# Kernel tuning notes

Hardware: AMD Instinct MI355X
Metric: run time of the kernel (lower is better)

## Reference

```python
import jax, jax.numpy as jnp
import numpy as np


def _make_constraint_mask(n=9):
    N = n * n
    rows = np.arange(N) // n
    cols = np.arange(N) % n
    box = (rows // 3) * 3 + cols // 3
    cm = np.stack([
        rows[:, None] == rows[None, :],
        cols[:, None] == cols[None, :],
        box[:, None] == box[None, :],
    ], axis=1).astype(np.float32)  # (N, 3, N)
    return cm


def setup_inputs() -> dict:
    n, H, B = 9, 100, 512
    N = n * n
    key = jax.random.key(0)
    k1, k2, k3, k4 = jax.random.split(key, 4)
    digits = jax.random.randint(k1, (B, N), 0, n)
    keep = jax.random.bernoulli(k2, 0.5, (B, N)).astype(jnp.float32)
    x = jax.nn.one_hot(digits, n, dtype=jnp.float32) * keep[..., None]
    constraint_mask = jnp.asarray(_make_constraint_mask(n))  # (81, 3, 81)
    W1 = jax.random.normal(k3, (H, 3 * n), jnp.float32) / np.sqrt(3 * n).astype(np.float32)
    W2 = jax.random.normal(k4, (n, H), jnp.float32) / np.sqrt(H).astype(np.float32)
    return {"x": x, "constraint_mask": constraint_mask, "W1": W1, "W2": W2}


def reference(x, constraint_mask, W1, W2):
    B, N, n = x.shape
    bidx = jnp.arange(B)

    def step(carry, _):
        x, x_pred = carry
        # sparse constraint aggregation: constraints[b,i,k,v] = sum_j cm[i,k,j] * x[b,j,v]
        constraints = jnp.einsum('ikj,bjv->bikv', constraint_mask, x)  # (B,N,3,n)
        empty = x.sum(-1) == 0  # (B,N) cells still unfilled
        f = constraints.reshape(B, N, 3 * n)
        s_ = jax.nn.softmax(jax.nn.relu(f @ W1.T) @ W2.T, axis=-1)  # (B,N,n)
        x_pred = jnp.where(empty[..., None], s_, x_pred)
        s = jnp.where(empty[..., None], s_, 0.0)
        score = s.max(-1)          # (B,N)
        pos = s.argmax(-1)         # (B,N) best digit per cell
        mmax = jnp.argmax(score, axis=1)  # (B,) most confident cell
        has_empty = empty.any(axis=1)     # rows with remaining empties get a write
        p = pos[bidx, mmax]
        old = x[bidx, mmax, p]
        x = x.at[bidx, mmax, p].set(jnp.where(has_empty, 1.0, old))
        return (x, x_pred), None

    # Original loops min_empty (= max empties in batch) times; iterations past a
    # row's fill point are exact no-ops, so a fixed N=n*n steps gives identical output.
    (x, x_pred), _ = jax.lax.scan(step, (x, x), None, length=N)
    return (x_pred, x)
```

## Files before the change

kernel.cpp:

```cpp
#include <hip/hip_runtime.h>
#include <math.h>


#define NCELL 81
#define ND 9
#define NH 100
#define NG 27
#define GP 12
#define NTHREADS 256

template<int OFF>
__device__ __forceinline__ float pt_dot(const float* __restrict__ gr,
                                        const float (&w1r)[NG], int bp)
{
    float g[9];
    float4 ga = *(const float4*)gr;
    float4 gb = *(const float4*)(gr + 4);
    g[0]=ga.x; g[1]=ga.y; g[2]=ga.z; g[3]=ga.w;
    g[4]=gb.x; g[5]=gb.y; g[6]=gb.z; g[7]=gb.w;
    g[8]=gr[8];
    float acc = 0.0f;
    #pragma unroll
    for (int v = 0; v < 9; ++v)
        acc = fmaf(w1r[OFF + v], g[v] + ((v == bp) ? 1.0f : 0.0f), acc);
    return acc;
}

__global__ __launch_bounds__(NTHREADS, 2)
void sudoku_solver_kernel(const float* __restrict__ x_in,
                          const float* __restrict__ W1,
                          const float* __restrict__ W2,
                          float* __restrict__ out,
                          int B)
{
    __shared__ float xs[NCELL * ND];
    __shared__ float xp[NCELL * ND];
    alignas(16) __shared__ float gsum[NG * GP];
    alignas(16) __shared__ float PT[NG * NH];
    alignas(16) __shared__ float hs[NCELL * NH];
    __shared__ float escore[NCELL];
    __shared__ int   epos[NCELL];
    __shared__ int   elist[NCELL];
    __shared__ int   wlist[NCELL];
    __shared__ int   EcntS, Wcnt;

    const int b   = blockIdx.x;
    const int tid = threadIdx.x;
    if (b >= B) return;

    const int lane = tid & 63;
    const int wv   = tid >> 6;
    const int sgrp = lane / 9;
    const int vd   = lane - 9 * sgrp;
    const int u    = tid % NH;
    const int sub  = tid / NH;

    float w1r[NG];
    if (tid < 2 * NH) {
        #pragma unroll
        for (int k = 0; k < NG; ++k) w1r[k] = W1[u * NG + k];
    }
    float4 w2r[25];
    {
        const float4* w2row = (const float4*)&W2[vd * NH];
        #pragma unroll
        for (int q = 0; q < 25; ++q) w2r[q] = w2row[q];
    }

    {
        const float* xb = x_in + (size_t)b * (NCELL * ND);
        for (int i = tid; i < NCELL * ND; i += NTHREADS) {
            float v = xb[i];
            xs[i] = v;
            xp[i] = v;
        }
    }
    if (tid == 0) EcntS = 0;
    __syncthreads();

    for (int t = tid; t < NCELL + NG * ND; t += NTHREADS) {
        if (t < NCELL) {
            const float* r = &xs[t * ND];
            float s = r[0]+r[1]+r[2]+r[3]+r[4]+r[5]+r[6]+r[7]+r[8];
            if (s == 0.0f) { int e = atomicAdd(&EcntS, 1); elist[e] = t; }
        } else {
            int g = (t - NCELL) / ND;
            int v = (t - NCELL) % ND;
            float acc = 0.0f;
            if (g < 9) {
                int base = g * 9;
                #pragma unroll
                for (int j = 0; j < 9; ++j) acc += xs[(base + j) * ND + v];
            } else if (g < 18) {
                int c = g - 9;
                #pragma unroll
                for (int j = 0; j < 9; ++j) acc += xs[(j * 9 + c) * ND + v];
            } else {
                int bb = g - 18;
                int br = (bb / 3) * 3, bc2 = (bb % 3) * 3;
                #pragma unroll
                for (int j = 0; j < 9; ++j)
                    acc += xs[((br + j / 3) * 9 + (bc2 + j % 3)) * ND + v];
            }
            gsum[g * GP + v] = acc;
        }
    }
    __syncthreads();

    int E_reg = EcntS;
    if (tid < 2 * NH) {
        for (int g = sub; g < NG; g += 2) {
            float acc;
            if (g < 9)       acc = pt_dot<0>(&gsum[g * GP], w1r, -1);
            else if (g < 18) acc = pt_dot<9>(&gsum[g * GP], w1r, -1);
            else             acc = pt_dot<18>(&gsum[g * GP], w1r, -1);
            PT[g * NH + u] = acc;
        }
    }
    for (int i = tid; i < E_reg; i += NTHREADS) wlist[i] = elist[i];
    __syncthreads();

    int W_reg = E_reg;
    int pend_cell = -1, pend_digit = 0, pend_be = 0;

    while (E_reg > 0) {
        if (tid == NTHREADS - 1) {
            Wcnt = 0;
            if (pend_cell >= 0) {
                int fr = pend_cell / 9, fc = pend_cell % 9;
                int fb = (fr / 3) * 3 + fc / 3;
                xs[pend_cell * ND + pend_digit] = 1.0f;
                gsum[fr * GP + pend_digit]        += 1.0f;
                gsum[(9 + fc) * GP + pend_digit]  += 1.0f;
                gsum[(18 + fb) * GP + pend_digit] += 1.0f;
                elist[pend_be] = elist[E_reg];
            }
        }
        for (int ch = tid; ch < W_reg * 25; ch += NTHREADS) {
            int wi = ch / 25, qc = ch - 25 * wi;
            int cell = wlist[wi];
            int r = cell / 9, c = cell - 9 * r;
            int bg = 18 + (r / 3) * 3 + c / 3;
            float4 hr = ((const float4*)&PT[r * NH])[qc];
            float4 hc = ((const float4*)&PT[(9 + c) * NH])[qc];
            float4 hb = ((const float4*)&PT[bg * NH])[qc];
            float4 h;
            h.x = fmaxf((hr.x + hc.x) + hb.x, 0.0f);
            h.y = fmaxf((hr.y + hc.y) + hb.y, 0.0f);
            h.z = fmaxf((hr.z + hc.z) + hb.z, 0.0f);
            h.w = fmaxf((hr.w + hc.w) + hb.w, 0.0f);
            ((float4*)&hs[wi * NH])[qc] = h;
        }
        __syncthreads();

        const int npass = (W_reg + 27) / 28;
        for (int pass = 0; pass < npass; ++pass) {
            int ci = pass * 28 + wv * 7 + sgrp;
            if (sgrp < 7 && ci < W_reg) {
                int cell = wlist[ci];
                const float4* h4 = (const float4*)&hs[ci * NH];
                float a0 = 0.0f, a1 = 0.0f;
                #pragma unroll
                for (int q = 0; q < 25; ++q) {
                    float4 hv = h4[q], w = w2r[q];
                    a0 = fmaf(w.x, hv.x, a0);
                    a0 = fmaf(w.y, hv.y, a0);
                    a1 = fmaf(w.z, hv.z, a1);
                    a1 = fmaf(w.w, hv.w, a1);
                }
                float l_own = a0 + a1;
                float l[9];
                #pragma unroll
                for (int j = 0; j < 9; ++j) l[j] = __shfl(l_own, 9 * sgrp + j, 64);
                float m = -INFINITY;
                #pragma unroll
                for (int j = 0; j < 9; ++j) m = fmaxf(m, l[j]);
                float e9[9]; float ss = 0.0f;
                #pragma unroll
                for (int j = 0; j < 9; ++j) { e9[j] = expf(l[j] - m); ss += e9[j]; }
                float best = -1.0f; int bp = 0; float svown = 0.0f;
                #pragma unroll
                for (int j = 0; j < 9; ++j) {
                    float sv = e9[j] / ss;
                    if (j == vd) svown = sv;
                    if (sv > best) { best = sv; bp = j; }
                }
                xp[cell * ND + vd] = svown;
                if (vd == 0) { escore[cell] = best; epos[cell] = bp; }
            }
        }
        __syncthreads();

        unsigned long long key = 0ULL;
        for (int e = lane; e < E_reg; e += 64) {
            int ce = elist[e];
            float sc = escore[ce];
            unsigned int lo = ((unsigned)(NCELL - ce) << 7) | (unsigned)e;
            unsigned long long k =
                ((unsigned long long)__float_as_uint(sc) << 32) | lo;
            if (k > key) key = k;
        }
        #pragma unroll
        for (int off = 32; off > 0; off >>= 1) {
            unsigned long long ok = __shfl_xor(key, off, 64);
            if (ok > key) key = ok;
        }
        const unsigned int lo = (unsigned int)key;
        const int bc = NCELL - (int)(lo >> 7);
        const int be = (int)(lo & 127);
        const int bp = epos[bc];
        const int fr = bc / 9, fc = bc % 9, fb = (fr / 3) * 3 + fc / 3;

        int Wn = 0;
        for (int base = 0; base < E_reg; base += 64) {
            int e = base + lane;
            bool pr = false;
            int ce = 0;
            if (e < E_reg && e != be) {
                ce = elist[e];
                int r = ce / 9, c = ce - 9 * r;
                pr = (r == fr) || (c == fc) || (((r / 3) * 3 + c / 3) == fb);
            }
            unsigned long long mask = __ballot(pr);
            Wn += (int)__popcll(mask);
            if (wv == 0 && pr) { int w = atomicAdd(&Wcnt, 1); wlist[w] = ce; }
        }

        if (tid < 2 * NH) {
            if (sub == 0) {
                PT[fr * NH + u]        = pt_dot<0>(&gsum[fr * GP], w1r, bp);
                PT[(18 + fb) * NH + u] = pt_dot<18>(&gsum[(18 + fb) * GP], w1r, bp);
            } else {
                PT[(9 + fc) * NH + u]  = pt_dot<9>(&gsum[(9 + fc) * GP], w1r, bp);
            }
        }

        E_reg -= 1;
        pend_cell = bc; pend_digit = bp; pend_be = be;
        W_reg = Wn;
        __syncthreads();
    }

    if (tid == NTHREADS - 1 && pend_cell >= 0)
        xs[pend_cell * ND + pend_digit] = 1.0f;
    __syncthreads();

    const size_t outb = (size_t)b * (NCELL * ND);
    const size_t half = (size_t)B * (NCELL * ND);
    for (int i = tid; i < NCELL * ND; i += NTHREADS) {
        out[outb + i]        = xp[i];
        out[half + outb + i] = xs[i];
    }
}

extern "C" void kernel_launch(void* const* d_in, const int* in_sizes, int n_in,
                              void* d_out, int out_size, void* d_ws, size_t ws_size,
                              hipStream_t stream)
{
    const float* x  = (const float*)d_in[0];
    const float* W1 = (const float*)d_in[2];
    const float* W2 = (const float*)d_in[3];
    float* out = (float*)d_out;
    const int B = in_sizes[0] / (NCELL * ND);

    sudoku_solver_kernel<<<dim3(B), dim3(NTHREADS), 0, stream>>>(x, W1, W2, out, B);
}
```

Measured before the change: 206.6 us.

## Remove per-step barrier by wave-local hidden compute and packed shared keys

The hidden-layer ReLU sums are now computed by the same wave that consumes them, which removes one block-wide barrier per solver step. Per-cell score, digit and index are packed into persistent 64-bit keys in shared memory, replacing the elist/escore/epos indirection and the list compaction. The write list is built with a ballot prefix instead of shared atomics. W2 moves from 25 float4 registers per thread into shared memory to lower register pressure, at the cost of extra LDS reads in the output dot product.

```diff
diff --git a/kernel.cpp b/kernel.cpp
--- a/kernel.cpp
+++ b/kernel.cpp
@@ -38,11 +38,11 @@
     alignas(16) __shared__ float gsum[NG * GP];
     alignas(16) __shared__ float PT[NG * NH];
     alignas(16) __shared__ float hs[NCELL * NH];
-    __shared__ float escore[NCELL];
-    __shared__ int   epos[NCELL];
-    __shared__ int   elist[NCELL];
-    __shared__ int   wlist[NCELL];
-    __shared__ int   EcntS, Wcnt;
+    alignas(16) __shared__ float W2s[ND * NH];
+    __shared__ unsigned long long pkey[NCELL];
+    __shared__ int ecell[NCELL];
+    __shared__ int wlist[NCELL];
+    __shared__ int EcntS;
 
     const int b   = blockIdx.x;
     const int tid = threadIdx.x;
@@ -60,13 +60,7 @@
         #pragma unroll
         for (int k = 0; k < NG; ++k) w1r[k] = W1[u * NG + k];
     }
-    float4 w2r[25];
-    {
-        const float4* w2row = (const float4*)&W2[vd * NH];
-        #pragma unroll
-        for (int q = 0; q < 25; ++q) w2r[q] = w2row[q];
-    }
-
+    for (int i = tid; i < ND * NH; i += NTHREADS) W2s[i] = W2[i];
     {
         const float* xb = x_in + (size_t)b * (NCELL * ND);
         for (int i = tid; i < NCELL * ND; i += NTHREADS) {
@@ -75,6 +69,7 @@
             xp[i] = v;
         }
     }
+    for (int i = tid; i < NCELL; i += NTHREADS) pkey[i] = 0ULL;
     if (tid == 0) EcntS = 0;
     __syncthreads();
 
@@ -82,7 +77,12 @@
         if (t < NCELL) {
             const float* r = &xs[t * ND];
             float s = r[0]+r[1]+r[2]+r[3]+r[4]+r[5]+r[6]+r[7]+r[8];
-            if (s == 0.0f) { int e = atomicAdd(&EcntS, 1); elist[e] = t; }
+            if (s == 0.0f) {
+                int e = atomicAdd(&EcntS, 1);
+                int rr = t / 9, cc = t % 9, bb = (rr / 3) * 3 + cc / 3;
+                ecell[e] = t | (rr << 8) | (cc << 12) | (bb << 16);
+                wlist[e] = t | (e << 8);
+            }
         } else {
             int g = (t - NCELL) / ND;
             int v = (t - NCELL) % ND;
@@ -107,7 +107,8 @@
     }
     __syncthreads();
 
-    int E_reg = EcntS;
+    int E_live = EcntS;
+    int W_reg  = E_live;
     if (tid < 2 * NH) {
         for (int g = sub; g < NG; g += 2) {
             float acc;
@@ -117,52 +118,52 @@
             PT[g * NH + u] = acc;
         }
     }
-    for (int i = tid; i < E_reg; i += NTHREADS) wlist[i] = elist[i];
-    __syncthreads();
-
-    int W_reg = E_reg;
+    __syncthreads();
+
     int pend_cell = -1, pend_digit = 0, pend_be = 0;
 
-    while (E_reg > 0) {
-        if (tid == NTHREADS - 1) {
-            Wcnt = 0;
-            if (pend_cell >= 0) {
-                int fr = pend_cell / 9, fc = pend_cell % 9;
-                int fb = (fr / 3) * 3 + fc / 3;
-                xs[pend_cell * ND + pend_digit] = 1.0f;
-                gsum[fr * GP + pend_digit]        += 1.0f;
-                gsum[(9 + fc) * GP + pend_digit]  += 1.0f;
-                gsum[(18 + fb) * GP + pend_digit] += 1.0f;
-                elist[pend_be] = elist[E_reg];
-            }
-        }
-        for (int ch = tid; ch < W_reg * 25; ch += NTHREADS) {
-            int wi = ch / 25, qc = ch - 25 * wi;
-            int cell = wlist[wi];
-            int r = cell / 9, c = cell - 9 * r;
-            int bg = 18 + (r / 3) * 3 + c / 3;
-            float4 hr = ((const float4*)&PT[r * NH])[qc];
-            float4 hc = ((const float4*)&PT[(9 + c) * NH])[qc];
-            float4 hb = ((const float4*)&PT[bg * NH])[qc];
-            float4 h;
-            h.x = fmaxf((hr.x + hc.x) + hb.x, 0.0f);
-            h.y = fmaxf((hr.y + hc.y) + hb.y, 0.0f);
-            h.z = fmaxf((hr.z + hc.z) + hb.z, 0.0f);
-            h.w = fmaxf((hr.w + hc.w) + hb.w, 0.0f);
-            ((float4*)&hs[wi * NH])[qc] = h;
-        }
-        __syncthreads();
-
-        const int npass = (W_reg + 27) / 28;
-        for (int pass = 0; pass < npass; ++pass) {
-            int ci = pass * 28 + wv * 7 + sgrp;
+    while (E_live > 0) {
+        if (tid == NTHREADS - 1 && pend_cell >= 0) {
+            int fr = pend_cell / 9, fc = pend_cell % 9;
+            int fb = (fr / 3) * 3 + fc / 3;
+            xs[pend_cell * ND + pend_digit] = 1.0f;
+            gsum[fr * GP + pend_digit]        += 1.0f;
+            gsum[(9 + fc) * GP + pend_digit]  += 1.0f;
+            gsum[(18 + fb) * GP + pend_digit] += 1.0f;
+            pkey[pend_be] = 0ULL;
+        }
+        const int npass  = (W_reg + 27) / 28;
+        const int nchunk = npass * 7 * 25;
+        for (int c = lane; c < nchunk; c += 64) {
+            int rl = c / 25, qc = c - 25 * rl;
+            int wi = (rl / 7) * 28 + wv * 7 + (rl % 7);
+            if (wi < W_reg) {
+                int cell = wlist[wi] & 255;
+                int r = cell / 9, cc2 = cell - 9 * r;
+                int bg = 18 + (r / 3) * 3 + cc2 / 3;
+                float4 hr = ((const float4*)&PT[r * NH])[qc];
+                float4 hc = ((const float4*)&PT[(9 + cc2) * NH])[qc];
+                float4 hb = ((const float4*)&PT[bg * NH])[qc];
+                float4 h;
+                h.x = fmaxf((hr.x + hc.x) + hb.x, 0.0f);
+                h.y = fmaxf((hr.y + hc.y) + hb.y, 0.0f);
+                h.z = fmaxf((hr.z + hc.z) + hb.z, 0.0f);
+                h.w = fmaxf((hr.w + hc.w) + hb.w, 0.0f);
+                ((float4*)&hs[wi * NH])[qc] = h;
+            }
+        }
+        for (int p = 0; p < npass; ++p) {
+            int ci = p * 28 + wv * 7 + sgrp;
             if (sgrp < 7 && ci < W_reg) {
-                int cell = wlist[ci];
+                int went = wlist[ci];
+                int cell = went & 255;
+                int we   = went >> 8;
                 const float4* h4 = (const float4*)&hs[ci * NH];
+                const float4* w4 = (const float4*)&W2s[vd * NH];
                 float a0 = 0.0f, a1 = 0.0f;
                 #pragma unroll
                 for (int q = 0; q < 25; ++q) {
-                    float4 hv = h4[q], w = w2r[q];
+                    float4 hv = h4[q], w = w4[q];
                     a0 = fmaf(w.x, hv.x, a0);
                     a0 = fmaf(w.y, hv.y, a0);
                     a1 = fmaf(w.z, hv.z, a1);
@@ -178,26 +179,24 @@
                 float e9[9]; float ss = 0.0f;
                 #pragma unroll
                 for (int j = 0; j < 9; ++j) { e9[j] = expf(l[j] - m); ss += e9[j]; }
-                float best = -1.0f; int bp = 0; float svown = 0.0f;
-                #pragma unroll
-                for (int j = 0; j < 9; ++j) {
-                    float sv = e9[j] / ss;
-                    if (j == vd) svown = sv;
-                    if (sv > best) { best = sv; bp = j; }
+                float bestE = -1.0f; int bp = 0;
+                #pragma unroll
+                for (int j = 0; j < 9; ++j)
+                    if (e9[j] > bestE) { bestE = e9[j]; bp = j; }
+                xp[cell * ND + vd] = e9[vd] / ss;
+                if (vd == 0) {
+                    float score = e9[bp] / ss;
+                    unsigned lo = ((unsigned)(NCELL - cell) << 11)
+                                | ((unsigned)bp << 7) | (unsigned)we;
+                    pkey[we] = ((unsigned long long)__float_as_uint(score) << 32) | lo;
                 }
-                xp[cell * ND + vd] = svown;
-                if (vd == 0) { escore[cell] = best; epos[cell] = bp; }
             }
         }
         __syncthreads();
 
         unsigned long long key = 0ULL;
-        for (int e = lane; e < E_reg; e += 64) {
-            int ce = elist[e];
-            float sc = escore[ce];
-            unsigned int lo = ((unsigned)(NCELL - ce) << 7) | (unsigned)e;
-            unsigned long long k =
-                ((unsigned long long)__float_as_uint(sc) << 32) | lo;
+        for (int e = lane; e < NCELL; e += 64) {
+            unsigned long long k = pkey[e];
             if (k > key) key = k;
         }
         #pragma unroll
@@ -205,25 +204,28 @@
             unsigned long long ok = __shfl_xor(key, off, 64);
             if (ok > key) key = ok;
         }
-        const unsigned int lo = (unsigned int)key;
-        const int bc = NCELL - (int)(lo >> 7);
+        const unsigned lo = (unsigned)key;
         const int be = (int)(lo & 127);
-        const int bp = epos[bc];
+        const int bp = (int)((lo >> 7) & 15);
+        const int bc = NCELL - (int)((lo >> 11) & 127);
         const int fr = bc / 9, fc = bc % 9, fb = (fr / 3) * 3 + fc / 3;
 
         int Wn = 0;
-        for (int base = 0; base < E_reg; base += 64) {
+        for (int base = 0; base < NCELL; base += 64) {
             int e = base + lane;
-            bool pr = false;
-            int ce = 0;
-            if (e < E_reg && e != be) {
-                ce = elist[e];
-                int r = ce / 9, c = ce - 9 * r;
-                pr = (r == fr) || (c == fc) || (((r / 3) * 3 + c / 3) == fb);
+            bool pr = false; int ce = 0;
+            if (e < NCELL && e != be && pkey[e] != 0ULL) {
+                int info = ecell[e];
+                ce = info & 255;
+                int r = (info >> 8) & 15, c = (info >> 12) & 15, bb = (info >> 16) & 15;
+                pr = (r == fr) || (c == fc) || (bb == fb);
             }
             unsigned long long mask = __ballot(pr);
+            if (wv == 0 && pr) {
+                int pos = Wn + (int)__popcll(mask & ((1ULL << lane) - 1ULL));
+                wlist[pos] = ce | (e << 8);
+            }
             Wn += (int)__popcll(mask);
-            if (wv == 0 && pr) { int w = atomicAdd(&Wcnt, 1); wlist[w] = ce; }
         }
 
         if (tid < 2 * NH) {
@@ -235,7 +237,7 @@
             }
         }
 
-        E_reg -= 1;
+        E_live -= 1;
         pend_cell = bc; pend_digit = bp; pend_be = be;
         W_reg = Wn;
         __syncthreads();
```

Result: slower. 235.6 us (+14.1%).
